# Kernel tuning notes

Hardware: AMD Instinct MI355X
Metric: run time of the kernel (lower is better)

## Reference

```python
import jax, jax.numpy as jnp
import numpy as np

N_HEADS = 4


def setup_inputs() -> dict:
    key = jax.random.key(0)
    ks = jax.random.split(key, 6)
    B, T, N, D = 4, 16, 64, 256
    x = jax.random.normal(ks[0], (B, T, N, D), dtype=jnp.float32)
    bias_features = jax.random.normal(ks[1], (B, T, N, N, D), dtype=jnp.float32)
    mask = jax.random.randint(ks[2], (B, T, N), 0, 2).astype(bool)
    s = 1.0 / np.sqrt(D).astype(np.float32)
    Wqkv = jax.random.normal(ks[3], (D, 3 * D), dtype=jnp.float32) * s
    bqkv = jnp.zeros((3 * D,), dtype=jnp.float32)
    Wproj = jax.random.normal(ks[4], (D, D), dtype=jnp.float32) * s
    bproj = jnp.zeros((D,), dtype=jnp.float32)
    return {"x": x, "bias_features": bias_features, "mask": mask,
            "Wqkv": Wqkv, "bqkv": bqkv, "Wproj": Wproj, "bproj": bproj}


def reference(x, bias_features, mask, Wqkv, bqkv, Wproj, bproj):
    B, T, N, D = x.shape
    H = N_HEADS
    hd = D // H
    Batch = B * T
    scale = 1.0 / float(np.sqrt(hd))

    x_flat = x.reshape(Batch, N, D)
    qkv = x_flat @ Wqkv + bqkv                      # (Batch, N, 3D)
    q, k, v = jnp.split(qkv, 3, axis=-1)
    q = q.reshape(Batch, N, H, hd).transpose(0, 2, 1, 3)   # (Batch, H, N, hd)
    k = k.reshape(Batch, N, H, hd).transpose(0, 2, 1, 3)
    v = v.reshape(Batch, N, H, hd).transpose(0, 2, 1, 3)

    # geometry bias: (Batch, H, N, N, hd)
    b_geo = bias_features.reshape(Batch, N, N, H, hd).transpose(0, 3, 1, 2, 4)
    # per-pair dot of q[n] with geometry feature for pair (n, m)
    rel_scores = jnp.einsum("bhnd,bhnmd->bhnm", q, b_geo) * scale

    mask_flat = mask.reshape(Batch, 1, 1, N)
    attn_bias = jnp.where(mask_flat, rel_scores, jnp.float32(-1e9))

    scores = jnp.einsum("bhnd,bhmd->bhnm", q, k) * scale + attn_bias
    attn = jax.nn.softmax(scores, axis=-1)
    out = jnp.einsum("bhnm,bhmd->bhnd", attn, v)    # (Batch, H, N, hd)

    out = out.transpose(0, 2, 1, 3).reshape(Batch, N, D)
    out = out @ Wproj + bproj
    return out.reshape(B, T, N, D)
```

## Files before the change

kernel.cpp:

```cpp
#include <hip/hip_runtime.h>
#include <hip/hip_bf16.h>

#define BATCH 64
#define NRES 64
#define DMODEL 256
#define ROWS (BATCH*NRES)
#define QKVC 768
#define SCALE 0.125f

__global__ __launch_bounds__(256) void qkv_gemm(
    const float* __restrict__ x, const float* __restrict__ W,
    const float* __restrict__ bq, float* __restrict__ qkv) {
  __shared__ float As[64 * 64];
  __shared__ float Bs[64 * 64];
  int t = threadIdx.x;
  int tx = t & 15, ty = t >> 4;
  int rowBase = blockIdx.y * 64;
  int colBase = blockIdx.x * 64;
  float acc[4][4] = {};
  for (int kb = 0; kb < 256; kb += 64) {
    for (int p = 0; p < 4; ++p) {
      int e = (p * 256 + t) * 4;
      int r = e >> 6, c = e & 63;
      *(float4*)&As[r * 64 + c] =
          *(const float4*)&x[(size_t)(rowBase + r) * 256 + kb + c];
      *(float4*)&Bs[r * 64 + c] =
          *(const float4*)&W[(size_t)(kb + r) * QKVC + colBase + c];
    }
    __syncthreads();
    for (int kk = 0; kk < 64; ++kk) {
      float a[4], b[4];
#pragma unroll
      for (int i = 0; i < 4; ++i) a[i] = As[(ty * 4 + i) * 64 + kk];
#pragma unroll
      for (int j = 0; j < 4; ++j) b[j] = Bs[kk * 64 + tx * 4 + j];
#pragma unroll
      for (int i = 0; i < 4; ++i)
#pragma unroll
        for (int j = 0; j < 4; ++j) acc[i][j] += a[i] * b[j];
    }
    __syncthreads();
  }
#pragma unroll
  for (int i = 0; i < 4; ++i) {
    int r = rowBase + ty * 4 + i;
#pragma unroll
    for (int j = 0; j < 4; ++j) {
      int c = colBase + tx * 4 + j;
      qkv[(size_t)r * QKVC + c] = acc[i][j] + bq[c];
    }
  }
}

__global__ __launch_bounds__(256) void qk_gemm(const float* __restrict__ qkv,
                                               float* __restrict__ qk) {
  __shared__ float qs[64 * 65];
  __shared__ float ks[64 * 65];
  int t = threadIdx.x;
  int bh = blockIdx.x;
  int b = bh >> 2, h = bh & 3;
  for (int i = 0; i < 16; ++i) {
    int idx = i * 256 + t;
    int r = idx >> 6, d = idx & 63;
    qs[r * 65 + d] = qkv[(size_t)(b * 64 + r) * QKVC + h * 64 + d];
    ks[r * 65 + d] = qkv[(size_t)(b * 64 + r) * QKVC + 256 + h * 64 + d];
  }
  __syncthreads();
  int m = t & 63, nq = t >> 6;
  for (int ni = 0; ni < 16; ++ni) {
    int n = nq * 16 + ni;
    float s = 0.f;
#pragma unroll 16
    for (int d = 0; d < 64; ++d) s += qs[n * 65 + d] * ks[m * 65 + d];
    qk[((size_t)bh * 64 + n) * 64 + m] = s;
  }
}

__global__ __launch_bounds__(256) void attn_kernel(
    const float* __restrict__ bias, const int* __restrict__ mask,
    const float* __restrict__ qkv, const float* __restrict__ qk,
    float* __restrict__ ctx) {
  __shared__ float q_s[256];
  __shared__ float rel_s[256];
  __shared__ float attn_s[256];
  int t = threadIdx.x;
  int blk = blockIdx.x;
  int b = blk >> 6;
  int n_res = blk & 63;
  q_s[t] = qkv[(size_t)blk * QKVC + t];
  __syncthreads();
  int wave = t >> 6, lane = t & 63;
  int hseg = lane >> 4;
  float4 qv = *(const float4*)&q_s[lane * 4];
  const float* brow_base = bias + (size_t)blk * 64 * 256;
  for (int i = 0; i < 16; ++i) {
    int m = i * 4 + wave;
    float4 bv = *(const float4*)&brow_base[(size_t)m * 256 + lane * 4];
    float p = bv.x * qv.x + bv.y * qv.y + bv.z * qv.z + bv.w * qv.w;
    p += __shfl_xor(p, 1, 64);
    p += __shfl_xor(p, 2, 64);
    p += __shfl_xor(p, 4, 64);
    p += __shfl_xor(p, 8, 64);
    if ((lane & 15) == 0) rel_s[hseg * 64 + m] = p;
  }
  __syncthreads();
  int m = t & 63, h = t >> 6;
  float rel = rel_s[h * 64 + m];
  float s_qk = qk[(((size_t)(b * 4 + h) * 64 + n_res) * 64) + m];
  float logit = s_qk * SCALE + (mask[b * 64 + m] ? rel * SCALE : -1e9f);
  float mx = logit;
#pragma unroll
  for (int off = 32; off > 0; off >>= 1) mx = fmaxf(mx, __shfl_xor(mx, off, 64));
  float ex = __expf(logit - mx);
  float sm = ex;
#pragma unroll
  for (int off = 32; off > 0; off >>= 1) sm += __shfl_xor(sm, off, 64);
  attn_s[h * 64 + m] = ex / sm;
  __syncthreads();
  int c = t;
  int hh = c >> 6;
  float acc = 0.f;
  const float* vbase = qkv + (size_t)b * 64 * QKVC + 512 + c;
#pragma unroll 8
  for (int mm = 0; mm < 64; ++mm) acc += attn_s[hh * 64 + mm] * vbase[(size_t)mm * QKVC];
  ctx[(size_t)blk * 256 + c] = acc;
}

__global__ __launch_bounds__(256) void proj_gemm(
    const float* __restrict__ ctx, const float* __restrict__ W,
    const float* __restrict__ bp, float* __restrict__ out) {
  __shared__ float As[64 * 64];
  __shared__ float Bs[64 * 64];
  int t = threadIdx.x;
  int tx = t & 15, ty = t >> 4;
  int rowBase = blockIdx.y * 64;
  int colBase = blockIdx.x * 64;
  float acc[4][4] = {};
  for (int kb = 0; kb < 256; kb += 64) {
    for (int p = 0; p < 4; ++p) {
      int e = (p * 256 + t) * 4;
      int r = e >> 6, c = e & 63;
      *(float4*)&As[r * 64 + c] =
          *(const float4*)&ctx[(size_t)(rowBase + r) * 256 + kb + c];
      *(float4*)&Bs[r * 64 + c] =
          *(const float4*)&W[(size_t)(kb + r) * 256 + colBase + c];
    }
    __syncthreads();
    for (int kk = 0; kk < 64; ++kk) {
      float a[4], bb[4];
#pragma unroll
      for (int i = 0; i < 4; ++i) a[i] = As[(ty * 4 + i) * 64 + kk];
#pragma unroll
      for (int j = 0; j < 4; ++j) bb[j] = Bs[kk * 64 + tx * 4 + j];
#pragma unroll
      for (int i = 0; i < 4; ++i)
#pragma unroll
        for (int j = 0; j < 4; ++j) acc[i][j] += a[i] * bb[j];
    }
    __syncthreads();
  }
#pragma unroll
  for (int i = 0; i < 4; ++i) {
    int r = rowBase + ty * 4 + i;
#pragma unroll
    for (int j = 0; j < 4; ++j) {
      int c = colBase + tx * 4 + j;
      out[(size_t)r * 256 + c] = acc[i][j] + bp[c];
    }
  }
}

extern "C" void kernel_launch(void* const* d_in, const int* in_sizes, int n_in,
                              void* d_out, int out_size, void* d_ws, size_t ws_size,
                              hipStream_t stream) {
  const float* x    = (const float*)d_in[0];
  const float* bias = (const float*)d_in[1];
  const int*   mask = (const int*)d_in[2];
  const float* Wqkv = (const float*)d_in[3];
  const float* bqkv = (const float*)d_in[4];
  const float* Wprj = (const float*)d_in[5];
  const float* bprj = (const float*)d_in[6];
  float* out = (float*)d_out;

  float* qkv_ws = (float*)d_ws;
  float* qk_ws  = qkv_ws + (size_t)ROWS * QKVC;
  float* ctx_ws = qk_ws + (size_t)BATCH * 4 * 64 * 64;

  qkv_gemm<<<dim3(12, 64), 256, 0, stream>>>(x, Wqkv, bqkv, qkv_ws);
  qk_gemm<<<256, 256, 0, stream>>>(qkv_ws, qk_ws);
  attn_kernel<<<ROWS, 256, 0, stream>>>(bias, mask, qkv_ws, qk_ws, ctx_ws);
  proj_gemm<<<dim3(4, 64), 256, 0, stream>>>(ctx_ws, Wprj, bprj, out);
}
```

Measured before the change: 438.7 us.

## Pad GEMM shared tiles, vectorize B loads, stream bias with nontemporal loads

```diff
diff --git a/kernel.cpp b/kernel.cpp
--- a/kernel.cpp
+++ b/kernel.cpp
@@ -7,33 +7,38 @@
 #define ROWS (BATCH*NRES)
 #define QKVC 768
 #define SCALE 0.125f
+#define LDP 68
+
+typedef float floatx4 __attribute__((ext_vector_type(4)));
 
 __global__ __launch_bounds__(256) void qkv_gemm(
     const float* __restrict__ x, const float* __restrict__ W,
     const float* __restrict__ bq, float* __restrict__ qkv) {
-  __shared__ float As[64 * 64];
-  __shared__ float Bs[64 * 64];
+  __shared__ float As[64 * LDP];
+  __shared__ float Bs[64 * LDP];
   int t = threadIdx.x;
   int tx = t & 15, ty = t >> 4;
   int rowBase = blockIdx.y * 64;
   int colBase = blockIdx.x * 64;
   float acc[4][4] = {};
   for (int kb = 0; kb < 256; kb += 64) {
+#pragma unroll
     for (int p = 0; p < 4; ++p) {
       int e = (p * 256 + t) * 4;
       int r = e >> 6, c = e & 63;
-      *(float4*)&As[r * 64 + c] =
+      *(float4*)&As[r * LDP + c] =
           *(const float4*)&x[(size_t)(rowBase + r) * 256 + kb + c];
-      *(float4*)&Bs[r * 64 + c] =
+      *(float4*)&Bs[r * LDP + c] =
           *(const float4*)&W[(size_t)(kb + r) * QKVC + colBase + c];
     }
     __syncthreads();
+#pragma unroll 4
     for (int kk = 0; kk < 64; ++kk) {
-      float a[4], b[4];
-#pragma unroll
-      for (int i = 0; i < 4; ++i) a[i] = As[(ty * 4 + i) * 64 + kk];
-#pragma unroll
-      for (int j = 0; j < 4; ++j) b[j] = Bs[kk * 64 + tx * 4 + j];
+      float a[4];
+      float4 b4 = *(const float4*)&Bs[kk * LDP + tx * 4];
+#pragma unroll
+      for (int i = 0; i < 4; ++i) a[i] = As[(ty * 4 + i) * LDP + kk];
+      float b[4] = {b4.x, b4.y, b4.z, b4.w};
 #pragma unroll
       for (int i = 0; i < 4; ++i)
 #pragma unroll
@@ -87,27 +92,30 @@
   int blk = blockIdx.x;
   int b = blk >> 6;
   int n_res = blk & 63;
+  int m = t & 63, h = t >> 6;
+  float s_qk = qk[(((size_t)(b * 4 + h) * 64 + n_res) * 64) + m];
+  int msk = mask[b * 64 + m];
   q_s[t] = qkv[(size_t)blk * QKVC + t];
   __syncthreads();
   int wave = t >> 6, lane = t & 63;
   int hseg = lane >> 4;
   float4 qv = *(const float4*)&q_s[lane * 4];
-  const float* brow_base = bias + (size_t)blk * 64 * 256;
+  const floatx4* brow_base =
+      (const floatx4*)(bias + (size_t)blk * 64 * 256);
+#pragma unroll 4
   for (int i = 0; i < 16; ++i) {
-    int m = i * 4 + wave;
-    float4 bv = *(const float4*)&brow_base[(size_t)m * 256 + lane * 4];
+    int mm = i * 4 + wave;
+    floatx4 bv = __builtin_nontemporal_load(&brow_base[mm * 64 + lane]);
     float p = bv.x * qv.x + bv.y * qv.y + bv.z * qv.z + bv.w * qv.w;
     p += __shfl_xor(p, 1, 64);
     p += __shfl_xor(p, 2, 64);
     p += __shfl_xor(p, 4, 64);
     p += __shfl_xor(p, 8, 64);
-    if ((lane & 15) == 0) rel_s[hseg * 64 + m] = p;
-  }
-  __syncthreads();
-  int m = t & 63, h = t >> 6;
+    if ((lane & 15) == 0) rel_s[hseg * 64 + mm] = p;
+  }
+  __syncthreads();
   float rel = rel_s[h * 64 + m];
-  float s_qk = qk[(((size_t)(b * 4 + h) * 64 + n_res) * 64) + m];
-  float logit = s_qk * SCALE + (mask[b * 64 + m] ? rel * SCALE : -1e9f);
+  float logit = s_qk * SCALE + (msk ? rel * SCALE : -1e9f);
   float mx = logit;
 #pragma unroll
   for (int off = 32; off > 0; off >>= 1) mx = fmaxf(mx, __shfl_xor(mx, off, 64));
@@ -129,33 +137,35 @@
 __global__ __launch_bounds__(256) void proj_gemm(
     const float* __restrict__ ctx, const float* __restrict__ W,
     const float* __restrict__ bp, float* __restrict__ out) {
-  __shared__ float As[64 * 64];
-  __shared__ float Bs[64 * 64];
+  __shared__ float As[64 * LDP];
+  __shared__ float Bs[64 * LDP];
   int t = threadIdx.x;
   int tx = t & 15, ty = t >> 4;
   int rowBase = blockIdx.y * 64;
   int colBase = blockIdx.x * 64;
   float acc[4][4] = {};
   for (int kb = 0; kb < 256; kb += 64) {
+#pragma unroll
     for (int p = 0; p < 4; ++p) {
       int e = (p * 256 + t) * 4;
       int r = e >> 6, c = e & 63;
-      *(float4*)&As[r * 64 + c] =
+      *(float4*)&As[r * LDP + c] =
           *(const float4*)&ctx[(size_t)(rowBase + r) * 256 + kb + c];
-      *(float4*)&Bs[r * 64 + c] =
+      *(float4*)&Bs[r * LDP + c] =
           *(const float4*)&W[(size_t)(kb + r) * 256 + colBase + c];
     }
     __syncthreads();
+#pragma unroll 4
     for (int kk = 0; kk < 64; ++kk) {
-      float a[4], bb[4];
-#pragma unroll
-      for (int i = 0; i < 4; ++i) a[i] = As[(ty * 4 + i) * 64 + kk];
-#pragma unroll
-      for (int j = 0; j < 4; ++j) bb[j] = Bs[kk * 64 + tx * 4 + j];
+      float a[4];
+      float4 b4 = *(const float4*)&Bs[kk * LDP + tx * 4];
+#pragma unroll
+      for (int i = 0; i < 4; ++i) a[i] = As[(ty * 4 + i) * LDP + kk];
+      float b[4] = {b4.x, b4.y, b4.z, b4.w};
 #pragma unroll
       for (int i = 0; i < 4; ++i)
 #pragma unroll
-        for (int j = 0; j < 4; ++j) acc[i][j] += a[i] * bb[j];
+        for (int j = 0; j < 4; ++j) acc[i][j] += a[i] * b[j];
     }
     __syncthreads();
   }
```

After: 407.4 us. 1.08x faster.
